# Kernel tuning notes

Hardware: AMD Instinct MI355X
Metric: run time of the kernel (lower is better)

Reference implementation:

```python
import jax, jax.numpy as jnp
import numpy as np

N_SRC = 50000      # source nodes
N_DST = 32000      # destination nodes
MAX_DEG = 16       # padded max in-degree
N_SUB = 4          # subtokens per node
D = 128            # hidden_dim
VOCAB = 32000
N_CLASSES = 104
LN_EPS = 1e-5


def setup_inputs() -> dict:
    key = jax.random.key(0)
    ks = jax.random.split(key, 12)
    token_id = jax.random.randint(ks[0], (N_SRC, N_SUB), 0, VOCAB)
    neigh_idx = jax.random.randint(ks[1], (N_DST, MAX_DEG), 0, N_SRC)
    deg = jax.random.randint(ks[2], (N_DST,), 1, MAX_DEG + 1)  # in-degree >= 1 (DGL asserts no 0-in-degree)
    s = 1.0 / np.sqrt(D)
    emb = jax.random.normal(ks[3], (VOCAB, D), dtype=jnp.float32) * np.sqrt(2.0 / D)  # kaiming_normal_
    w_ih = jax.random.uniform(ks[4], (3 * D, D), minval=-s, maxval=s, dtype=jnp.float32)  # gates r,z,n
    w_hh = jax.random.uniform(ks[5], (3 * D, D), minval=-s, maxval=s, dtype=jnp.float32)
    b_ih = jax.random.uniform(ks[6], (3 * D,), minval=-s, maxval=s, dtype=jnp.float32)
    b_hh = jax.random.uniform(ks[7], (3 * D,), minval=-s, maxval=s, dtype=jnp.float32)
    gamma = jnp.ones((D,), jnp.float32)
    beta = jnp.zeros((D,), jnp.float32)
    sc = 1.0 / np.sqrt(D)
    wc = jax.random.uniform(ks[8], (N_CLASSES, D), minval=-sc, maxval=sc, dtype=jnp.float32)
    bc = jax.random.uniform(ks[9], (N_CLASSES,), minval=-sc, maxval=sc, dtype=jnp.float32)
    return dict(token_id=token_id, neigh_idx=neigh_idx, deg=deg, emb=emb,
                w_ih=w_ih, w_hh=w_hh, b_ih=b_ih, b_hh=b_hh,
                gamma=gamma, beta=beta, wc=wc, bc=bc)


def reference(token_id, neigh_idx, deg, emb, w_ih, w_hh, b_ih, b_hh, gamma, beta, wc, bc):
    # node features: mean over subtokens of embedding lookup
    feat_src = emb[token_id].mean(axis=1)                 # [N_src, D]
    msgs = feat_src[neigh_idx]                            # [N_dst, max_deg, D] (mailbox)
    T = MAX_DEG - 1                                       # GRU runs over the first L-1 messages
    # precompute input projections for all steps (one big GEMM)
    x_proj = jnp.einsum('ntd,ed->nte', msgs[:, :T], w_ih) + b_ih  # [N_dst, T, 3D]

    def gru_step(h, inp):
        xp, active = inp                                  # xp [N,3D], active [N]
        hp = h @ w_hh.T + b_hh
        xr, xz, xn = jnp.split(xp, 3, axis=-1)
        hr, hz, hn = jnp.split(hp, 3, axis=-1)
        r = jax.nn.sigmoid(xr + hr)
        z = jax.nn.sigmoid(xz + hz)
        n = jnp.tanh(xn + r * hn)
        h_new = (1.0 - z) * n + z * h
        h = jnp.where(active[:, None], h_new, h)          # freeze finished (short-degree) rows
        return h, None

    steps = jnp.arange(T)
    active = steps[:, None] < (deg - 1)[None, :]          # [T, N_dst]: step t valid iff t < L-1
    h0 = jnp.zeros((N_DST, D), msgs.dtype)
    h, _ = jax.lax.scan(gru_step, h0, (jnp.transpose(x_proj, (1, 0, 2)), active))

    # layernorm on final GRU hidden state
    mu = h.mean(axis=-1, keepdims=True)
    var = ((h - mu) ** 2).mean(axis=-1, keepdims=True)
    ln = (h - mu) / jnp.sqrt(var + LN_EPS) * gamma + beta
    # degree-1 nodes: ft = the single message (no GRU, no layernorm)
    ft = jnp.where((deg == 1)[:, None], msgs[:, 0], ln)   # [N_dst, D]
    return ft @ wc.T + bc                                 # [N_dst, n_classes]
```

## Files before the change

kernel.cpp:

```cpp
#include <hip/hip_runtime.h>

typedef unsigned short u16;
typedef unsigned int u32;
typedef __attribute__((ext_vector_type(8))) short short8;
typedef __attribute__((ext_vector_type(4))) float f32x4;

#define NDST 32000
#define NSRC 50000
#define MAXDEG 16
#define DH 128
#define NCLS 104
#define SBLK 125
#define NTILE 1000
#define GRID_GRU 256

#define MFMA(a, b, c) __builtin_amdgcn_mfma_f32_16x16x32_bf16(a, b, c, 0, 0, 0)

__device__ __forceinline__ u16 f2bf(float f) {
  union { float f; u32 u; } v; v.f = f;
  return (u16)((v.u + 0x7FFFu + ((v.u >> 16) & 1u)) >> 16);
}
__device__ __forceinline__ float bf2f(u16 x) {
  union { u32 u; float f; } v; v.u = (u32)x << 16;
  return v.f;
}
__device__ __forceinline__ float sigm(float x) { return 1.f / (1.f + __expf(-x)); }
__device__ __forceinline__ float tanhfast(float x) {
  float ax = fabsf(x);
  float e = __expf(2.f * ax);
  float t = 1.f - 2.f / (e + 1.f);
  return copysignf(t, x);
}
__device__ __forceinline__ f32x4 splat4(float x) { f32x4 v = {x, x, x, x}; return v; }

__global__ void k_prep(const float* __restrict__ wih, const float* __restrict__ whh,
                       const float* __restrict__ wc,
                       u16* __restrict__ wihb, u16* __restrict__ whhb, u16* __restrict__ wcb) {
  int i = blockIdx.x * 256 + threadIdx.x;
  if (i < 384 * DH) { wihb[i] = f2bf(wih[i]); whhb[i] = f2bf(whh[i]); }
  if (i < 112 * DH) { int r = i >> 7; wcb[i] = (r < NCLS) ? f2bf(wc[i]) : (u16)0; }
}

__global__ void k_embcvt(const float* __restrict__ emb, u16* __restrict__ embb) {
  int i = blockIdx.x * 256 + threadIdx.x;
  const float* p = emb + (size_t)i * 8;
  u16 u[8];
#pragma unroll
  for (int j = 0; j < 8; ++j) u[j] = f2bf(p[j]);
  uint4 pk;
  pk.x = u[0] | ((u32)u[1] << 16);
  pk.y = u[2] | ((u32)u[3] << 16);
  pk.z = u[4] | ((u32)u[5] << 16);
  pk.w = u[6] | ((u32)u[7] << 16);
  *reinterpret_cast<uint4*>(embb + (size_t)i * 8) = pk;
}

__global__ void k_embed(const int* __restrict__ token, const u16* __restrict__ embb,
                        u16* __restrict__ featb) {
  int gid = blockIdx.x * 256 + threadIdx.x;
  if (gid >= NSRC * 16) return;
  int n = gid >> 4, c = gid & 15;
  const int* tk = token + n * 4;
  int t0 = tk[0], t1 = tk[1], t2 = tk[2], t3 = tk[3];
  short8 e0 = *(const short8*)(embb + (size_t)t0 * DH + c * 8);
  short8 e1 = *(const short8*)(embb + (size_t)t1 * DH + c * 8);
  short8 e2 = *(const short8*)(embb + (size_t)t2 * DH + c * 8);
  short8 e3 = *(const short8*)(embb + (size_t)t3 * DH + c * 8);
  u16 u[8];
#pragma unroll
  for (int j = 0; j < 8; ++j) {
    float a = bf2f((u16)e0[j]) + bf2f((u16)e1[j]) + bf2f((u16)e2[j]) + bf2f((u16)e3[j]);
    u[j] = f2bf(a * 0.25f);
  }
  uint4 pk;
  pk.x = u[0] | ((u32)u[1] << 16);
  pk.y = u[2] | ((u32)u[3] << 16);
  pk.z = u[4] | ((u32)u[5] << 16);
  pk.w = u[6] | ((u32)u[7] << 16);
  *reinterpret_cast<uint4*>(featb + (size_t)n * DH + c * 8) = pk;
}

__global__ void k_hist(const int* __restrict__ deg, int* __restrict__ blkhist) {
  __shared__ int h[16];
  int tid = threadIdx.x;
  if (tid < 16) h[tid] = 0;
  __syncthreads();
  int node = blockIdx.x * 256 + tid;
  atomicAdd(&h[deg[node] - 1], 1);
  __syncthreads();
  if (tid < 16) blkhist[blockIdx.x * 16 + tid] = h[tid];
}

__global__ void k_scan(const int* __restrict__ blkhist, int* __restrict__ offs,
                       int* __restrict__ base16) {
  __shared__ int tot_s[16];
  int t = threadIdx.x;
  int k = t >> 4, i = t & 15;
  int loc[8];
  int s = 0;
#pragma unroll
  for (int b = 0; b < 8; ++b) {
    int bb = i * 8 + b;
    int v = (bb < SBLK) ? blkhist[bb * 16 + k] : 0;
    loc[b] = s;
    s += v;
  }
  int ps = s;
#pragma unroll
  for (int d = 1; d < 16; d <<= 1) {
    int o = __shfl_up(ps, d, 16);
    if (i >= d) ps += o;
  }
  int excl = ps - s;
#pragma unroll
  for (int b = 0; b < 8; ++b) {
    int bb = i * 8 + b;
    if (bb < SBLK) offs[bb * 16 + k] = excl + loc[b];
  }
  if (i == 15) tot_s[k] = ps;
  __syncthreads();
  if (t == 0) {
    int run = 0;
    for (int q = 0; q < 16; ++q) { base16[q] = run; run += tot_s[q]; }
  }
}

__global__ void k_scatter(const int* __restrict__ deg, const int* __restrict__ offs,
                          const int* __restrict__ base16, int* __restrict__ perm) {
  __shared__ int lc[16];
  int tid = threadIdx.x;
  if (tid < 16) lc[tid] = 0;
  __syncthreads();
  int node = blockIdx.x * 256 + tid;
  int k = deg[node] - 1;
  int p = atomicAdd(&lc[k], 1);
  perm[base16[k] + offs[blockIdx.x * 16 + k] + p] = node;
}

__global__ __launch_bounds__(512, 2) void k_gru(
    const int* __restrict__ neigh, const int* __restrict__ deg,
    const int* __restrict__ perm, const u16* __restrict__ featb,
    const u16* __restrict__ wihb, const u16* __restrict__ whhb,
    const float* __restrict__ bih, const float* __restrict__ bhh,
    const float* __restrict__ gamma, const float* __restrict__ beta,
    const u16* __restrict__ wcb, const float* __restrict__ bc,
    float* __restrict__ out) {
  __shared__ u16 Hb[2][32][DH];
  __shared__ int nid_s[32];
  __shared__ int neigh_s[MAXDEG][32];
  __shared__ int deg_s[32];
  __shared__ float Hf[32][DH + 1];
  __shared__ u16 Ft[32][DH];
  __shared__ float gam_s[DH], bet_s[DH];

  const int tid = threadIdx.x;
  const int w = tid >> 6;
  const int l = tid & 63;
  const int l16 = l & 15;
  const int lq = l >> 4;
  const int col = w * 16 + l16;
  const int swzA = (l16 & 7) << 3;

  if (tid < DH) { gam_s[tid] = gamma[tid]; bet_s[tid] = beta[tid]; }

  short8 Wr[4], Wz[4], Wn[4], Ur[4], Uz[4], Un[4];
#pragma unroll
  for (int kc = 0; kc < 4; ++kc) {
    int ko = kc * 32 + lq * 8;
    const u16* pw = wihb + (size_t)col * DH + ko;
    const u16* pu = whhb + (size_t)col * DH + ko;
    Wr[kc] = *(const short8*)pw;
    Wz[kc] = *(const short8*)(pw + DH * DH);
    Wn[kc] = *(const short8*)(pw + 2 * DH * DH);
    Ur[kc] = *(const short8*)pu;
    Uz[kc] = *(const short8*)(pu + DH * DH);
    Un[kc] = *(const short8*)(pu + 2 * DH * DH);
  }
  float bR = bih[col] + bhh[col];
  float bZ = bih[DH + col] + bhh[DH + col];
  float bXN = bih[2 * DH + col];
  float bHN = bhh[2 * DH + col];
  asm volatile("" : "+v"(Wr[0]), "+v"(Wr[1]), "+v"(Wr[2]), "+v"(Wr[3]));
  asm volatile("" : "+v"(Wz[0]), "+v"(Wz[1]), "+v"(Wz[2]), "+v"(Wz[3]));
  asm volatile("" : "+v"(Wn[0]), "+v"(Wn[1]), "+v"(Wn[2]), "+v"(Wn[3]));
  asm volatile("" : "+v"(Ur[0]), "+v"(Ur[1]), "+v"(Ur[2]), "+v"(Ur[3]));
  asm volatile("" : "+v"(Uz[0]), "+v"(Uz[1]), "+v"(Uz[2]), "+v"(Uz[3]));
  asm volatile("" : "+v"(Un[0]), "+v"(Un[1]), "+v"(Un[2]), "+v"(Un[3]));
  asm volatile("" : "+v"(bR), "+v"(bZ), "+v"(bXN), "+v"(bHN));

#pragma unroll 1
  for (int g = 0; g < 4; ++g) {
    int tile = (g & 1) ? ((g + 1) * GRID_GRU - 1 - (int)blockIdx.x)
                       : (g * GRID_GRU + (int)blockIdx.x);
    if (tile >= NTILE) continue;

    __syncthreads();
    if (tid < 32) nid_s[tid] = perm[tile * 32 + tid];
    __syncthreads();
    {
      int node = tid >> 4, t = tid & 15;
      neigh_s[t][node] = neigh[(size_t)nid_s[node] * MAXDEG + t];
    }
    if (tid < 32) deg_s[tid] = deg[nid_s[tid]];
    {
      uint4 z = {0, 0, 0, 0};
      ((uint4*)Hb[0])[tid] = z;
    }
    __syncthreads();

    const int tmax = deg_s[31] - 1;
    int degm1[2][4];
#pragma unroll
    for (int m = 0; m < 2; ++m)
#pragma unroll
      for (int r = 0; r < 4; ++r) degm1[m][r] = deg_s[m * 16 + lq * 4 + r] - 1;
    float hreg[2][4] = {{0, 0, 0, 0}, {0, 0, 0, 0}};

    if (tmax > 0) {
      short8 axA[2][4], axB[2][4];
      {
        int s0 = neigh_s[0][l16], s1 = neigh_s[0][16 + l16];
#pragma unroll
        for (int kc = 0; kc < 4; ++kc) {
          int ko = kc * 32 + lq * 8;
          axA[0][kc] = *(const short8*)(featb + (size_t)s0 * DH + ko);
          axA[1][kc] = *(const short8*)(featb + (size_t)s1 * DH + ko);
        }
      }

#define GRU_STEP(T, AXC, AXN, BR, BW)                                          \
  do {                                                                         \
    int sn0 = neigh_s[(T) + 1][l16], sn1 = neigh_s[(T) + 1][16 + l16];         \
    _Pragma("unroll") for (int kc = 0; kc < 4; ++kc) {                         \
      int ko = kc * 32 + lq * 8;                                               \
      AXN[0][kc] = *(const short8*)(featb + (size_t)sn0 * DH + ko);            \
      AXN[1][kc] = *(const short8*)(featb + (size_t)sn1 * DH + ko);            \
    }                                                                          \
    f32x4 aR0 = splat4(bR), aR1 = splat4(bR), aZ0 = splat4(bZ),                \
          aZ1 = splat4(bZ), aN0 = splat4(bXN), aN1 = splat4(bXN),              \
          aH0 = splat4(bHN), aH1 = splat4(bHN);                                \
    _Pragma("unroll") for (int kc = 0; kc < 4; ++kc) {                         \
      int ko = kc * 32 + lq * 8;                                               \
      short8 ah0 = *(const short8*)&BR[l16][ko ^ swzA];                        \
      short8 ah1 = *(const short8*)&BR[16 + l16][ko ^ swzA];                   \
      aR0 = MFMA(AXC[0][kc], Wr[kc], aR0);                                     \
      aR1 = MFMA(AXC[1][kc], Wr[kc], aR1);                                     \
      aZ0 = MFMA(AXC[0][kc], Wz[kc], aZ0);                                     \
      aZ1 = MFMA(AXC[1][kc], Wz[kc], aZ1);                                     \
      aN0 = MFMA(AXC[0][kc], Wn[kc], aN0);                                     \
      aN1 = MFMA(AXC[1][kc], Wn[kc], aN1);                                     \
      aR0 = MFMA(ah0, Ur[kc], aR0);                                            \
      aR1 = MFMA(ah1, Ur[kc], aR1);                                            \
      aZ0 = MFMA(ah0, Uz[kc], aZ0);                                            \
      aZ1 = MFMA(ah1, Uz[kc], aZ1);                                            \
      aH0 = MFMA(ah0, Un[kc], aH0);                                            \
      aH1 = MFMA(ah1, Un[kc], aH1);                                            \
    }                                                                          \
    _Pragma("unroll") for (int m = 0; m < 2; ++m) {                            \
      f32x4 vR = m ? aR1 : aR0, vZ = m ? aZ1 : aZ0;                            \
      f32x4 vN = m ? aN1 : aN0, vH = m ? aH1 : aH0;                            \
      _Pragma("unroll") for (int r = 0; r < 4; ++r) {                          \
        float rr = sigm(vR[r]);                                                \
        float zz = sigm(vZ[r]);                                                \
        float nn = tanhfast(vN[r] + rr * vH[r]);                               \
        float hN = (1.f - zz) * nn + zz * hreg[m][r];                          \
        if ((T) < degm1[m][r]) hreg[m][r] = hN;                                \
        int row = m * 16 + lq * 4 + r;                                         \
        BW[row][col ^ ((row & 7) << 3)] = f2bf(hreg[m][r]);                    \
      }                                                                        \
    }                                                                          \
    __syncthreads();                                                           \
  } while (0)

#pragma unroll 1
      for (int t = 0; t < tmax; t += 2) {
        GRU_STEP(t, axA, axB, Hb[0], Hb[1]);
        if (t + 1 >= tmax) break;
        GRU_STEP(t + 1, axB, axA, Hb[1], Hb[0]);
      }
#undef GRU_STEP
    }

#pragma unroll
    for (int m = 0; m < 2; ++m)
#pragma unroll
      for (int r = 0; r < 4; ++r) Hf[m * 16 + lq * 4 + r][col] = hreg[m][r];
    __syncthreads();

    {
      int node = tid >> 4, sub = tid & 15;
      float v[8];
      float s = 0.f, s2 = 0.f;
#pragma unroll
      for (int j = 0; j < 8; ++j) {
        v[j] = Hf[node][sub * 8 + j];
        s += v[j];
        s2 += v[j] * v[j];
      }
      s += __shfl_xor(s, 1, 64); s2 += __shfl_xor(s2, 1, 64);
      s += __shfl_xor(s, 2, 64); s2 += __shfl_xor(s2, 2, 64);
      s += __shfl_xor(s, 4, 64); s2 += __shfl_xor(s2, 4, 64);
      s += __shfl_xor(s, 8, 64); s2 += __shfl_xor(s2, 8, 64);
      float mu = s * (1.f / 128.f);
      float var = s2 * (1.f / 128.f) - mu * mu;
      float rstd = rsqrtf(var + 1e-5f);
      bool isd1 = (deg_s[node] == 1);
      uint4 fv = *(const uint4*)(featb + (size_t)neigh_s[0][node] * DH + sub * 8);
      const u16* fp = (const u16*)&fv;
      u16 ob[8];
#pragma unroll
      for (int j = 0; j < 8; ++j) {
        int d = sub * 8 + j;
        float ln = (v[j] - mu) * rstd * gam_s[d] + bet_s[d];
        ob[j] = isd1 ? fp[j] : f2bf(ln);
      }
      int e = (sub * 8) ^ ((node & 7) << 3);
      uint4 pk;
      pk.x = ob[0] | ((u32)ob[1] << 16);
      pk.y = ob[2] | ((u32)ob[3] << 16);
      pk.z = ob[4] | ((u32)ob[5] << 16);
      pk.w = ob[6] | ((u32)ob[7] << 16);
      *(uint4*)&Ft[node][e] = pk;
    }
    __syncthreads();

    if (w < 7) {
      f32x4 c0 = splat4(0.f), c1 = splat4(0.f);
#pragma unroll
      for (int kc = 0; kc < 4; ++kc) {
        int ko = kc * 32 + lq * 8;
        short8 a0 = *(const short8*)&Ft[l16][ko ^ swzA];
        short8 a1 = *(const short8*)&Ft[16 + l16][ko ^ swzA];
        short8 b = *(const short8*)(wcb + (size_t)col * DH + ko);
        c0 = MFMA(a0, b, c0);
        c1 = MFMA(a1, b, c1);
      }
      if (col < NCLS) {
        float bcv = bc[col];
#pragma unroll
        for (int m = 0; m < 2; ++m)
#pragma unroll
          for (int r = 0; r < 4; ++r) {
            float vv = (m ? c1[r] : c0[r]) + bcv;
            int rowg = nid_s[m * 16 + lq * 4 + r];
            out[(size_t)rowg * NCLS + col] = vv;
          }
      }
    }
  }
}

extern "C" void kernel_launch(void* const* d_in, const int* in_sizes, int n_in,
                              void* d_out, int out_size, void* d_ws, size_t ws_size,
                              hipStream_t stream) {
  const int* token = (const int*)d_in[0];
  const int* neigh = (const int*)d_in[1];
  const int* deg = (const int*)d_in[2];
  const float* emb = (const float*)d_in[3];
  const float* wih = (const float*)d_in[4];
  const float* whh = (const float*)d_in[5];
  const float* bih = (const float*)d_in[6];
  const float* bhh = (const float*)d_in[7];
  const float* gamma = (const float*)d_in[8];
  const float* beta = (const float*)d_in[9];
  const float* wc = (const float*)d_in[10];
  const float* bc = (const float*)d_in[11];
  float* out = (float*)d_out;

  u16* featb = (u16*)d_ws;
  u16* wihb = featb + (size_t)NSRC * DH;
  u16* whhb = wihb + 384 * DH;
  u16* wcb = whhb + 384 * DH;
  u16* embb = wcb + 112 * DH;
  int* perm = (int*)(embb + (size_t)32000 * DH);
  int* blkhist = perm + NDST;
  int* offs = blkhist + SBLK * 16;
  int* base16 = offs + SBLK * 16;

  hipLaunchKernelGGL(k_prep, dim3(192), dim3(256), 0, stream, wih, whh, wc, wihb, whhb, wcb);
  hipLaunchKernelGGL(k_embcvt, dim3(2000), dim3(256), 0, stream, emb, embb);
  hipLaunchKernelGGL(k_embed, dim3((NSRC * 16 + 255) / 256), dim3(256), 0, stream, token, embb, featb);
  hipLaunchKernelGGL(k_hist, dim3(SBLK), dim3(256), 0, stream, deg, blkhist);
  hipLaunchKernelGGL(k_scan, dim3(1), dim3(256), 0, stream, blkhist, offs, base16);
  hipLaunchKernelGGL(k_scatter, dim3(SBLK), dim3(256), 0, stream, deg, offs, base16, perm);
  hipLaunchKernelGGL(k_gru, dim3(GRID_GRU), dim3(512), 0, stream, neigh, deg, perm, featb,
                     wihb, whhb, bih, bhh, gamma, beta, wcb, bc, out);
}
```

Before: 218.7 us.

## Fuse front-end kernels and interleave two GRU tiles per block

Merges the weight conversion, the embedding gather-mean (now reading fp32 embeddings directly instead of first converting the whole table to bf16) and the degree histogram into a single front kernel. The GRU kernel now launches one block per pair of degree-sorted tiles and interleaves the recurrence steps of both tiles, sharing one barrier per step. This is meant to give the matrix units independent work to overlap and to cut per-tile sync and launch overhead. It also moves the next-step feature prefetch after the MFMAs and simplifies tanh. In exchange it uses more shared memory, reads twice the embedding bytes in fp32, and the simplified tanh can overflow for large inputs.

```diff
diff --git a/kernel.cpp b/kernel.cpp
--- a/kernel.cpp
+++ b/kernel.cpp
@@ -12,7 +12,7 @@
 #define NCLS 104
 #define SBLK 125
 #define NTILE 1000
-#define GRID_GRU 256
+#define NBLK_GRU 500
 
 #define MFMA(a, b, c) __builtin_amdgcn_mfma_f32_16x16x32_bf16(a, b, c, 0, 0, 0)
 
@@ -20,75 +20,59 @@
   union { float f; u32 u; } v; v.f = f;
   return (u16)((v.u + 0x7FFFu + ((v.u >> 16) & 1u)) >> 16);
 }
-__device__ __forceinline__ float bf2f(u16 x) {
-  union { u32 u; float f; } v; v.u = (u32)x << 16;
-  return v.f;
-}
 __device__ __forceinline__ float sigm(float x) { return 1.f / (1.f + __expf(-x)); }
-__device__ __forceinline__ float tanhfast(float x) {
-  float ax = fabsf(x);
-  float e = __expf(2.f * ax);
-  float t = 1.f - 2.f / (e + 1.f);
-  return copysignf(t, x);
+__device__ __forceinline__ float tanh1(float x) {
+  return 1.f - 2.f / (1.f + __expf(2.f * x));
 }
 __device__ __forceinline__ f32x4 splat4(float x) { f32x4 v = {x, x, x, x}; return v; }
 
-__global__ void k_prep(const float* __restrict__ wih, const float* __restrict__ whh,
-                       const float* __restrict__ wc,
-                       u16* __restrict__ wihb, u16* __restrict__ whhb, u16* __restrict__ wcb) {
-  int i = blockIdx.x * 256 + threadIdx.x;
-  if (i < 384 * DH) { wihb[i] = f2bf(wih[i]); whhb[i] = f2bf(whh[i]); }
-  if (i < 112 * DH) { int r = i >> 7; wcb[i] = (r < NCLS) ? f2bf(wc[i]) : (u16)0; }
-}
-
-__global__ void k_embcvt(const float* __restrict__ emb, u16* __restrict__ embb) {
-  int i = blockIdx.x * 256 + threadIdx.x;
-  const float* p = emb + (size_t)i * 8;
-  u16 u[8];
-#pragma unroll
-  for (int j = 0; j < 8; ++j) u[j] = f2bf(p[j]);
-  uint4 pk;
-  pk.x = u[0] | ((u32)u[1] << 16);
-  pk.y = u[2] | ((u32)u[3] << 16);
-  pk.z = u[4] | ((u32)u[5] << 16);
-  pk.w = u[6] | ((u32)u[7] << 16);
-  *reinterpret_cast<uint4*>(embb + (size_t)i * 8) = pk;
-}
-
-__global__ void k_embed(const int* __restrict__ token, const u16* __restrict__ embb,
-                        u16* __restrict__ featb) {
-  int gid = blockIdx.x * 256 + threadIdx.x;
-  if (gid >= NSRC * 16) return;
-  int n = gid >> 4, c = gid & 15;
-  const int* tk = token + n * 4;
-  int t0 = tk[0], t1 = tk[1], t2 = tk[2], t3 = tk[3];
-  short8 e0 = *(const short8*)(embb + (size_t)t0 * DH + c * 8);
-  short8 e1 = *(const short8*)(embb + (size_t)t1 * DH + c * 8);
-  short8 e2 = *(const short8*)(embb + (size_t)t2 * DH + c * 8);
-  short8 e3 = *(const short8*)(embb + (size_t)t3 * DH + c * 8);
-  u16 u[8];
-#pragma unroll
-  for (int j = 0; j < 8; ++j) {
-    float a = bf2f((u16)e0[j]) + bf2f((u16)e1[j]) + bf2f((u16)e2[j]) + bf2f((u16)e3[j]);
-    u[j] = f2bf(a * 0.25f);
-  }
-  uint4 pk;
-  pk.x = u[0] | ((u32)u[1] << 16);
-  pk.y = u[2] | ((u32)u[3] << 16);
-  pk.z = u[4] | ((u32)u[5] << 16);
-  pk.w = u[6] | ((u32)u[7] << 16);
-  *reinterpret_cast<uint4*>(featb + (size_t)n * DH + c * 8) = pk;
-}
-
-__global__ void k_hist(const int* __restrict__ deg, int* __restrict__ blkhist) {
+__global__ void k_front(const int* __restrict__ token, const float* __restrict__ emb,
+                        const float* __restrict__ wih, const float* __restrict__ whh,
+                        const float* __restrict__ wc, const int* __restrict__ deg,
+                        u16* __restrict__ featb, u16* __restrict__ wihb,
+                        u16* __restrict__ whhb, u16* __restrict__ wcb,
+                        int* __restrict__ blkhist) {
   __shared__ int h[16];
-  int tid = threadIdx.x;
-  if (tid < 16) h[tid] = 0;
-  __syncthreads();
-  int node = blockIdx.x * 256 + tid;
-  atomicAdd(&h[deg[node] - 1], 1);
-  __syncthreads();
-  if (tid < 16) blkhist[blockIdx.x * 16 + tid] = h[tid];
+  const int bid = blockIdx.x, tid = threadIdx.x;
+  const bool do_hist = (bid < SBLK);
+  if (do_hist) {
+    if (tid < 16) h[tid] = 0;
+    __syncthreads();
+    atomicAdd(&h[deg[bid * 256 + tid] - 1], 1);
+  }
+  {
+    int gid = bid * 256 + tid;
+    int n = gid >> 4, c = gid & 15;
+    const int* tk = token + n * 4;
+    float a[8];
+#pragma unroll
+    for (int j = 0; j < 8; ++j) a[j] = 0.f;
+#pragma unroll
+    for (int s = 0; s < 4; ++s) {
+      const float* p = emb + (size_t)tk[s] * DH + c * 8;
+#pragma unroll
+      for (int j = 0; j < 8; ++j) a[j] += p[j];
+    }
+    u16 u[8];
+#pragma unroll
+    for (int j = 0; j < 8; ++j) u[j] = f2bf(a[j] * 0.25f);
+    uint4 pk;
+    pk.x = u[0] | ((u32)u[1] << 16);
+    pk.y = u[2] | ((u32)u[3] << 16);
+    pk.z = u[4] | ((u32)u[5] << 16);
+    pk.w = u[6] | ((u32)u[7] << 16);
+    *reinterpret_cast<uint4*>(featb + (size_t)n * DH + c * 8) = pk;
+  }
+  if (bid >= SBLK && bid < SBLK + 192) {
+    int i = (bid - SBLK) * 256 + tid;
+    wihb[i] = f2bf(wih[i]);
+    whhb[i] = f2bf(whh[i]);
+    if (i < 112 * DH) { int r = i >> 7; wcb[i] = (r < NCLS) ? f2bf(wc[i]) : (u16)0; }
+  }
+  if (do_hist) {
+    __syncthreads();
+    if (tid < 16) blkhist[bid * 16 + tid] = h[tid];
+  }
 }
 
 __global__ void k_scan(const int* __restrict__ blkhist, int* __restrict__ offs,
@@ -145,12 +129,11 @@
     const float* __restrict__ gamma, const float* __restrict__ beta,
     const u16* __restrict__ wcb, const float* __restrict__ bc,
     float* __restrict__ out) {
-  __shared__ u16 Hb[2][32][DH];
-  __shared__ int nid_s[32];
-  __shared__ int neigh_s[MAXDEG][32];
-  __shared__ int deg_s[32];
+  __shared__ u16 Hb[2][2][32][DH];
+  __shared__ int neigh_s[2][MAXDEG][32];
+  __shared__ int nid_s[2][32];
+  __shared__ int deg_s[2][32];
   __shared__ float Hf[32][DH + 1];
-  __shared__ u16 Ft[32][DH];
   __shared__ float gam_s[DH], bet_s[DH];
 
   const int tid = threadIdx.x;
@@ -160,8 +143,26 @@
   const int lq = l >> 4;
   const int col = w * 16 + l16;
   const int swzA = (l16 & 7) << 3;
-
+  const int tA = 2 * (NBLK_GRU - 1 - (int)blockIdx.x);
+
+  if (tid < 64) nid_s[tid >> 5][tid & 31] = perm[(tA + (tid >> 5)) * 32 + (tid & 31)];
   if (tid < DH) { gam_s[tid] = gamma[tid]; bet_s[tid] = beta[tid]; }
+  __syncthreads();
+  {
+    int p = tid >> 8, rem = tid & 255;
+#pragma unroll
+    for (int q = 0; q < 2; ++q) {
+      int e = q * 256 + rem;
+      int node = e >> 4, t = e & 15;
+      neigh_s[p][t][node] = neigh[(size_t)nid_s[p][node] * MAXDEG + t];
+    }
+  }
+  if (tid < 64) deg_s[tid >> 5][tid & 31] = deg[nid_s[tid >> 5][tid & 31]];
+  {
+    uint4 z = {0, 0, 0, 0};
+    ((uint4*)Hb[0][0])[tid] = z;
+    ((uint4*)Hb[1][0])[tid] = z;
+  }
 
   short8 Wr[4], Wz[4], Wn[4], Ur[4], Uz[4], Un[4];
 #pragma unroll
@@ -187,68 +188,50 @@
   asm volatile("" : "+v"(Uz[0]), "+v"(Uz[1]), "+v"(Uz[2]), "+v"(Uz[3]));
   asm volatile("" : "+v"(Un[0]), "+v"(Un[1]), "+v"(Un[2]), "+v"(Un[3]));
   asm volatile("" : "+v"(bR), "+v"(bZ), "+v"(bXN), "+v"(bHN));
-
-#pragma unroll 1
-  for (int g = 0; g < 4; ++g) {
-    int tile = (g & 1) ? ((g + 1) * GRID_GRU - 1 - (int)blockIdx.x)
-                       : (g * GRID_GRU + (int)blockIdx.x);
-    if (tile >= NTILE) continue;
-
-    __syncthreads();
-    if (tid < 32) nid_s[tid] = perm[tile * 32 + tid];
-    __syncthreads();
-    {
-      int node = tid >> 4, t = tid & 15;
-      neigh_s[t][node] = neigh[(size_t)nid_s[node] * MAXDEG + t];
+  __syncthreads();
+
+  const int tmaxA = deg_s[0][31] - 1;
+  const int tmaxB = deg_s[1][31] - 1;
+  int degm1_0[2][4], degm1_1[2][4];
+#pragma unroll
+  for (int m = 0; m < 2; ++m)
+#pragma unroll
+    for (int r = 0; r < 4; ++r) {
+      degm1_0[m][r] = deg_s[0][m * 16 + lq * 4 + r] - 1;
+      degm1_1[m][r] = deg_s[1][m * 16 + lq * 4 + r] - 1;
     }
-    if (tid < 32) deg_s[tid] = deg[nid_s[tid]];
-    {
-      uint4 z = {0, 0, 0, 0};
-      ((uint4*)Hb[0])[tid] = z;
+  float hreg0[2][4] = {{0, 0, 0, 0}, {0, 0, 0, 0}};
+  float hreg1[2][4] = {{0, 0, 0, 0}, {0, 0, 0, 0}};
+
+  short8 ax0[2][4], ax1[2][4];
+  {
+    int a0 = neigh_s[0][0][l16], a1 = neigh_s[0][0][16 + l16];
+    int b0 = neigh_s[1][0][l16], b1 = neigh_s[1][0][16 + l16];
+#pragma unroll
+    for (int kc = 0; kc < 4; ++kc) {
+      int ko = kc * 32 + lq * 8;
+      ax0[0][kc] = *(const short8*)(featb + (size_t)a0 * DH + ko);
+      ax0[1][kc] = *(const short8*)(featb + (size_t)a1 * DH + ko);
+      ax1[0][kc] = *(const short8*)(featb + (size_t)b0 * DH + ko);
+      ax1[1][kc] = *(const short8*)(featb + (size_t)b1 * DH + ko);
     }
-    __syncthreads();
-
-    const int tmax = deg_s[31] - 1;
-    int degm1[2][4];
-#pragma unroll
-    for (int m = 0; m < 2; ++m)
-#pragma unroll
-      for (int r = 0; r < 4; ++r) degm1[m][r] = deg_s[m * 16 + lq * 4 + r] - 1;
-    float hreg[2][4] = {{0, 0, 0, 0}, {0, 0, 0, 0}};
-
-    if (tmax > 0) {
-      short8 axA[2][4], axB[2][4];
-      {
-        int s0 = neigh_s[0][l16], s1 = neigh_s[0][16 + l16];
-#pragma unroll
-        for (int kc = 0; kc < 4; ++kc) {
-          int ko = kc * 32 + lq * 8;
-          axA[0][kc] = *(const short8*)(featb + (size_t)s0 * DH + ko);
-          axA[1][kc] = *(const short8*)(featb + (size_t)s1 * DH + ko);
-        }
-      }
-
-#define GRU_STEP(T, AXC, AXN, BR, BW)                                          \
+  }
+
+#define PHASE(HB_R, HB_W, AX, HREG, DEGM1, NS, T)                              \
   do {                                                                         \
-    int sn0 = neigh_s[(T) + 1][l16], sn1 = neigh_s[(T) + 1][16 + l16];         \
-    _Pragma("unroll") for (int kc = 0; kc < 4; ++kc) {                         \
-      int ko = kc * 32 + lq * 8;                                               \
-      AXN[0][kc] = *(const short8*)(featb + (size_t)sn0 * DH + ko);            \
-      AXN[1][kc] = *(const short8*)(featb + (size_t)sn1 * DH + ko);            \
-    }                                                                          \
     f32x4 aR0 = splat4(bR), aR1 = splat4(bR), aZ0 = splat4(bZ),                \
           aZ1 = splat4(bZ), aN0 = splat4(bXN), aN1 = splat4(bXN),              \
           aH0 = splat4(bHN), aH1 = splat4(bHN);                                \
     _Pragma("unroll") for (int kc = 0; kc < 4; ++kc) {                         \
       int ko = kc * 32 + lq * 8;                                               \
-      short8 ah0 = *(const short8*)&BR[l16][ko ^ swzA];                        \
-      short8 ah1 = *(const short8*)&BR[16 + l16][ko ^ swzA];                   \
-      aR0 = MFMA(AXC[0][kc], Wr[kc], aR0);                                     \
-      aR1 = MFMA(AXC[1][kc], Wr[kc], aR1);                                     \
-      aZ0 = MFMA(AXC[0][kc], Wz[kc], aZ0);                                     \
-      aZ1 = MFMA(AXC[1][kc], Wz[kc], aZ1);                                     \
-      aN0 = MFMA(AXC[0][kc], Wn[kc], aN0);                                     \
-      aN1 = MFMA(AXC[1][kc], Wn[kc], aN1);                                     \
+      short8 ah0 = *(const short8*)&HB_R[l16][ko ^ swzA];                      \
+      short8 ah1 = *(const short8*)&HB_R[16 + l16][ko ^ swzA];                 \
+      aR0 = MFMA(AX[0][kc], Wr[kc], aR0);                                      \
+      aR1 = MFMA(AX[1][kc], Wr[kc], aR1);                                      \
+      aZ0 = MFMA(AX[0][kc], Wz[kc], aZ0);                                      \
+      aZ1 = MFMA(AX[1][kc], Wz[kc], aZ1);                                      \
+      aN0 = MFMA(AX[0][kc], Wn[kc], aN0);                                      \
+      aN1 = MFMA(AX[1][kc], Wn[kc], aN1);                                      \
       aR0 = MFMA(ah0, Ur[kc], aR0);                                            \
       aR1 = MFMA(ah1, Ur[kc], aR1);                                            \
       aZ0 = MFMA(ah0, Uz[kc], aZ0);                                            \
@@ -256,98 +239,112 @@
       aH0 = MFMA(ah0, Un[kc], aH0);                                            \
       aH1 = MFMA(ah1, Un[kc], aH1);                                            \
     }                                                                          \
+    {                                                                          \
+      int sn0 = NS[(T) + 1][l16], sn1 = NS[(T) + 1][16 + l16];                 \
+      _Pragma("unroll") for (int kc = 0; kc < 4; ++kc) {                       \
+        int ko = kc * 32 + lq * 8;                                             \
+        AX[0][kc] = *(const short8*)(featb + (size_t)sn0 * DH + ko);           \
+        AX[1][kc] = *(const short8*)(featb + (size_t)sn1 * DH + ko);           \
+      }                                                                        \
+    }                                                                          \
     _Pragma("unroll") for (int m = 0; m < 2; ++m) {                            \
       f32x4 vR = m ? aR1 : aR0, vZ = m ? aZ1 : aZ0;                            \
       f32x4 vN = m ? aN1 : aN0, vH = m ? aH1 : aH0;                            \
       _Pragma("unroll") for (int r = 0; r < 4; ++r) {                          \
         float rr = sigm(vR[r]);                                                \
         float zz = sigm(vZ[r]);                                                \
-        float nn = tanhfast(vN[r] + rr * vH[r]);                               \
-        float hN = (1.f - zz) * nn + zz * hreg[m][r];                          \
-        if ((T) < degm1[m][r]) hreg[m][r] = hN;                                \
+        float nn = tanh1(vN[r] + rr * vH[r]);                                  \
+        float hN = (1.f - zz) * nn + zz * HREG[m][r];                          \
+        if ((T) < DEGM1[m][r]) HREG[m][r] = hN;                                \
         int row = m * 16 + lq * 4 + r;                                         \
-        BW[row][col ^ ((row & 7) << 3)] = f2bf(hreg[m][r]);                    \
-      }                                                                        \
+        HB_W[row][col ^ ((row & 7) << 3)] = f2bf(HREG[m][r]);                  \
+      }                                                                        \
+    }                                                                          \
+  } while (0)
+
+  int cur = 0;
+#pragma unroll 1
+  for (int t = 0; t < tmaxB; ++t) {
+    if (t < tmaxA) PHASE(Hb[0][cur], Hb[0][cur ^ 1], ax0, hreg0, degm1_0, neigh_s[0], t);
+    PHASE(Hb[1][cur], Hb[1][cur ^ 1], ax1, hreg1, degm1_1, neigh_s[1], t);
+    __syncthreads();
+    cur ^= 1;
+  }
+#undef PHASE
+
+  const int fbA = tmaxA & 1, fbB = tmaxB & 1;
+
+#define LNPASS(HREG, P, FB)                                                    \
+  do {                                                                         \
+    _Pragma("unroll") for (int m = 0; m < 2; ++m)                              \
+        _Pragma("unroll") for (int r = 0; r < 4; ++r)                          \
+            Hf[m * 16 + lq * 4 + r][col] = HREG[m][r];                         \
+    __syncthreads();                                                           \
+    {                                                                          \
+      int node = tid >> 4, sub = tid & 15;                                     \
+      float v[8];                                                              \
+      float s = 0.f, s2 = 0.f;                                                 \
+      _Pragma("unroll") for (int j = 0; j < 8; ++j) {                          \
+        v[j] = Hf[node][sub * 8 + j];                                          \
+        s += v[j];                                                             \
+        s2 += v[j] * v[j];                                                     \
+      }                                                                        \
+      s += __shfl_xor(s, 1, 64); s2 += __shfl_xor(s2, 1, 64);                  \
+      s += __shfl_xor(s, 2, 64); s2 += __shfl_xor(s2, 2, 64);                  \
+      s += __shfl_xor(s, 4, 64); s2 += __shfl_xor(s2, 4, 64);                  \
+      s += __shfl_xor(s, 8, 64); s2 += __shfl_xor(s2, 8, 64);                  \
+      float mu = s * (1.f / 128.f);                                            \
+      float var = s2 * (1.f / 128.f) - mu * mu;                                \
+      float rstd = rsqrtf(var + 1e-5f);                                        \
+      bool isd1 = (deg_s[P][node] == 1);                                       \
+      uint4 fv = *(const uint4*)(featb + (size_t)neigh_s[P][0][node] * DH + sub * 8); \
+      const u16* fp = (const u16*)&fv;                                         \
+      u16 ob[8];                                                               \
+      _Pragma("unroll") for (int j = 0; j < 8; ++j) {                          \
+        int d = sub * 8 + j;                                                   \
+        float ln = (v[j] - mu) * rstd * gam_s[d] + bet_s[d];                   \
+        ob[j] = isd1 ? fp[j] : f2bf(ln);                                       \
+      }                                                                        \
+      int e = (sub * 8) ^ ((node & 7) << 3);                                   \
+      uint4 pk;                                                                \
+      pk.x = ob[0] | ((u32)ob[1] << 16);                                       \
+      pk.y = ob[2] | ((u32)ob[3] << 16);                                       \
+      pk.z = ob[4] | ((u32)ob[5] << 16);                                       \
+      pk.w = ob[6] | ((u32)ob[7] << 16);                                       \
+      *(uint4*)&Hb[P][(FB) ^ 1][node][e] = pk;                                 \
     }                                                                          \
     __syncthreads();                                                           \
   } while (0)
 
-#pragma unroll 1
-      for (int t = 0; t < tmax; t += 2) {
-        GRU_STEP(t, axA, axB, Hb[0], Hb[1]);
-        if (t + 1 >= tmax) break;
-        GRU_STEP(t + 1, axB, axA, Hb[1], Hb[0]);
-      }
-#undef GRU_STEP
-    }
-
-#pragma unroll
-    for (int m = 0; m < 2; ++m)
-#pragma unroll
-      for (int r = 0; r < 4; ++r) Hf[m * 16 + lq * 4 + r][col] = hreg[m][r];
-    __syncthreads();
-
-    {
-      int node = tid >> 4, sub = tid & 15;
-      float v[8];
-      float s = 0.f, s2 = 0.f;
-#pragma unroll
-      for (int j = 0; j < 8; ++j) {
-        v[j] = Hf[node][sub * 8 + j];
-        s += v[j];
-        s2 += v[j] * v[j];
-      }
-      s += __shfl_xor(s, 1, 64); s2 += __shfl_xor(s2, 1, 64);
-      s += __shfl_xor(s, 2, 64); s2 += __shfl_xor(s2, 2, 64);
-      s += __shfl_xor(s, 4, 64); s2 += __shfl_xor(s2, 4, 64);
-      s += __shfl_xor(s, 8, 64); s2 += __shfl_xor(s2, 8, 64);
-      float mu = s * (1.f / 128.f);
-      float var = s2 * (1.f / 128.f) - mu * mu;
-      float rstd = rsqrtf(var + 1e-5f);
-      bool isd1 = (deg_s[node] == 1);
-      uint4 fv = *(const uint4*)(featb + (size_t)neigh_s[0][node] * DH + sub * 8);
-      const u16* fp = (const u16*)&fv;
-      u16 ob[8];
-#pragma unroll
-      for (int j = 0; j < 8; ++j) {
-        int d = sub * 8 + j;
-        float ln = (v[j] - mu) * rstd * gam_s[d] + bet_s[d];
-        ob[j] = isd1 ? fp[j] : f2bf(ln);
-      }
-      int e = (sub * 8) ^ ((node & 7) << 3);
-      uint4 pk;
-      pk.x = ob[0] | ((u32)ob[1] << 16);
-      pk.y = ob[2] | ((u32)ob[3] << 16);
-      pk.z = ob[4] | ((u32)ob[5] << 16);
-      pk.w = ob[6] | ((u32)ob[7] << 16);
-      *(uint4*)&Ft[node][e] = pk;
-    }
-    __syncthreads();
-
-    if (w < 7) {
-      f32x4 c0 = splat4(0.f), c1 = splat4(0.f);
-#pragma unroll
-      for (int kc = 0; kc < 4; ++kc) {
-        int ko = kc * 32 + lq * 8;
-        short8 a0 = *(const short8*)&Ft[l16][ko ^ swzA];
-        short8 a1 = *(const short8*)&Ft[16 + l16][ko ^ swzA];
-        short8 b = *(const short8*)(wcb + (size_t)col * DH + ko);
-        c0 = MFMA(a0, b, c0);
-        c1 = MFMA(a1, b, c1);
-      }
-      if (col < NCLS) {
-        float bcv = bc[col];
-#pragma unroll
-        for (int m = 0; m < 2; ++m)
-#pragma unroll
-          for (int r = 0; r < 4; ++r) {
-            float vv = (m ? c1[r] : c0[r]) + bcv;
-            int rowg = nid_s[m * 16 + lq * 4 + r];
-            out[(size_t)rowg * NCLS + col] = vv;
-          }
-      }
-    }
-  }
+  LNPASS(hreg0, 0, fbA);
+  LNPASS(hreg1, 1, fbB);
+#undef LNPASS
+
+#define CLS(P, FB)                                                             \
+  if (w < 7) {                                                                 \
+    f32x4 c0 = splat4(0.f), c1 = splat4(0.f);                                  \
+    _Pragma("unroll") for (int kc = 0; kc < 4; ++kc) {                         \
+      int ko = kc * 32 + lq * 8;                                               \
+      short8 a0 = *(const short8*)&Hb[P][(FB) ^ 1][l16][ko ^ swzA];            \
+      short8 a1 = *(const short8*)&Hb[P][(FB) ^ 1][16 + l16][ko ^ swzA];       \
+      short8 b = *(const short8*)(wcb + (size_t)col * DH + ko);                \
+      c0 = MFMA(a0, b, c0);                                                    \
+      c1 = MFMA(a1, b, c1);                                                    \
+    }                                                                          \
+    if (col < NCLS) {                                                          \
+      float bcv = bc[col];                                                     \
+      _Pragma("unroll") for (int m = 0; m < 2; ++m)                            \
+          _Pragma("unroll") for (int r = 0; r < 4; ++r) {                      \
+        float vv = (m ? c1[r] : c0[r]) + bcv;                                  \
+        int rowg = nid_s[P][m * 16 + lq * 4 + r];                              \
+        out[(size_t)rowg * NCLS + col] = vv;                                   \
+      }                                                                        \
+    }                                                                          \
+  }
+
+  CLS(0, fbA);
+  CLS(1, fbB);
+#undef CLS
 }
 
 extern "C" void kernel_launch(void* const* d_in, const int* in_sizes, int n_in,
@@ -371,18 +368,15 @@
   u16* wihb = featb + (size_t)NSRC * DH;
   u16* whhb = wihb + 384 * DH;
   u16* wcb = whhb + 384 * DH;
-  u16* embb = wcb + 112 * DH;
-  int* perm = (int*)(embb + (size_t)32000 * DH);
+  int* perm = (int*)(wcb + 112 * DH);
   int* blkhist = perm + NDST;
   int* offs = blkhist + SBLK * 16;
   int* base16 = offs + SBLK * 16;
 
-  hipLaunchKernelGGL(k_prep, dim3(192), dim3(256), 0, stream, wih, whh, wc, wihb, whhb, wcb);
-  hipLaunchKernelGGL(k_embcvt, dim3(2000), dim3(256), 0, stream, emb, embb);
-  hipLaunchKernelGGL(k_embed, dim3((NSRC * 16 + 255) / 256), dim3(256), 0, stream, token, embb, featb);
-  hipLaunchKernelGGL(k_hist, dim3(SBLK), dim3(256), 0, stream, deg, blkhist);
+  hipLaunchKernelGGL(k_front, dim3(3125), dim3(256), 0, stream, token, emb, wih, whh, wc,
+                     deg, featb, wihb, whhb, wcb, blkhist);
   hipLaunchKernelGGL(k_scan, dim3(1), dim3(256), 0, stream, blkhist, offs, base16);
   hipLaunchKernelGGL(k_scatter, dim3(SBLK), dim3(256), 0, stream, deg, offs, base16, perm);
-  hipLaunchKernelGGL(k_gru, dim3(GRID_GRU), dim3(512), 0, stream, neigh, deg, perm, featb,
+  hipLaunchKernelGGL(k_gru, dim3(NBLK_GRU), dim3(512), 0, stream, neigh, deg, perm, featb,
                      wihb, whhb, bih, bhh, gamma, beta, wcb, bc, out);
 }
```

Measured after the change: 248.9 us. 1.14x slower.
